# Kernel optimization log

Measured on AMD Instinct MI355X. Metric: run time of the kernel, lower is better.

Reference implementation:

```python
import jax, jax.numpy as jnp
import numpy as np

B, N, E, H, DEPTH = 2, 2048, 1024, 8, 12
D = E // H // 2  # head_dim = 64
LN_EPS = 1e-5


def setup_inputs() -> dict:
    key = jax.random.key(0)
    ks = jax.random.split(key, 10)
    w = lambda k: jax.random.normal(k, (E, E), jnp.float32) * (E ** -0.5)
    lp = lambda k: jax.random.normal(k, (D,), jnp.float32) * 0.1
    return {
        "x": jax.random.normal(ks[0], (B, N, E), jnp.float32),
        "Wq": w(ks[1]), "Wk": w(ks[2]), "Wv": w(ks[3]), "Wo": w(ks[4]),
        "lq1": lp(ks[5]), "lk1": lp(ks[6]), "lq2": lp(ks[7]), "lk2": lp(ks[8]),
        "ln_g": jnp.ones((2 * D,), jnp.float32),
        "ln_b": jnp.zeros((2 * D,), jnp.float32),
    }


def reference(x, Wq, Wk, Wv, Wo, lq1, lk1, lq2, lk2, ln_g, ln_b):
    b, n, e = x.shape
    lam_init = 0.8 - 0.6 * np.exp(-0.3 * DEPTH)  # lambda_init_fn(depth)
    # projections; split into 2H half-heads of dim D for q,k; H heads of dim 2D for v
    q = (x @ Wq).reshape(b, n, 2 * H, D).transpose(0, 2, 1, 3) * (D ** -0.5)  # [b,2H,n,D]
    k = (x @ Wk).reshape(b, n, 2 * H, D).transpose(0, 2, 1, 3)                # [b,2H,n,D]
    v = (x @ Wv).reshape(b, n, H, 2 * D).transpose(0, 2, 1, 3)                # [b,H,n,2D]
    scores = jnp.einsum('bhqd,bhkd->bhqk', q, k)                              # [b,2H,n,n]
    attn = jax.nn.softmax(scores, axis=-1).reshape(b, H, 2, n, n)
    lam = jnp.exp(jnp.sum(lq1 * lk1)) - jnp.exp(jnp.sum(lq2 * lk2)) + lam_init
    w_diff = attn[:, :, 0] - lam * attn[:, :, 1]                              # [b,H,n,n]
    o = jnp.einsum('bhqk,bhkd->bhqd', w_diff, v)                              # [b,H,n,2D]
    # per-head LayerNorm over channel dim 2D
    mu = o.mean(-1, keepdims=True)
    var = ((o - mu) ** 2).mean(-1, keepdims=True)
    o = (o - mu) * jax.lax.rsqrt(var + LN_EPS) * ln_g + ln_b
    o = o.transpose(0, 2, 1, 3).reshape(b, n, e)
    return o @ Wo
```

## Files before the change

### kernel.cpp

```cpp
#include <hip/hip_runtime.h>
#include <hip/hip_bf16.h>
#include <math.h>

#define B_ 2
#define N_ 2048
#define E_ 1024
#define H_ 8

typedef __attribute__((ext_vector_type(8))) short frag8;
typedef __attribute__((ext_vector_type(4))) float f32x4;
typedef __attribute__((ext_vector_type(16))) float f32x16;
typedef __attribute__((ext_vector_type(8))) unsigned short u16x8;

constexpr float LAM_INIT = 0.7836057665316245f;
constexpr float LOG2E = 1.4426950408889634f;
constexpr float EXP2_GUARD = -23.083120654f;

static __device__ __forceinline__ float fast_exp2(float x) {
#if __has_builtin(__builtin_amdgcn_exp2f)
  return __builtin_amdgcn_exp2f(x);
#else
  return exp2f(x);
#endif
}

static __device__ __forceinline__ ushort f2bf(float f) {
  union { float f; unsigned u; } v; v.f = f;
  unsigned r = (v.u + 0x7FFFu + ((v.u >> 16) & 1u)) >> 16;
  return (ushort)r;
}

static __device__ __forceinline__ unsigned pkbf(float a, float b) {
  __hip_bfloat162 h = __float22bfloat162_rn(make_float2(a, b));
  return *(unsigned*)&h;
}

static __device__ __forceinline__ void async16(const void* g, void* l) {
  __builtin_amdgcn_global_load_lds((const __attribute__((address_space(1))) void*)g,
                                   (__attribute__((address_space(3))) void*)l, 16, 0, 0);
}

static __device__ __forceinline__ frag8 mkfrag(unsigned p0, unsigned p1,
                                               unsigned p2, unsigned p3) {
  auto r02 = __builtin_amdgcn_permlane32_swap((int)p0, (int)p2, false, false);
  auto r13 = __builtin_amdgcn_permlane32_swap((int)p1, (int)p3, false, false);
  union { unsigned u[4]; frag8 f; } u;
  u.u[0] = (unsigned)r02[0];
  u.u[1] = (unsigned)r13[0];
  u.u[2] = (unsigned)r02[1];
  u.u[3] = (unsigned)r13[1];
  return u.f;
}

__global__ __launch_bounds__(256) void prep_kernel(
    const float* __restrict__ x,
    const float* __restrict__ Wq, const float* __restrict__ Wk,
    const float* __restrict__ Wv, const float* __restrict__ Wo,
    const float* __restrict__ lq1, const float* __restrict__ lk1,
    const float* __restrict__ lq2, const float* __restrict__ lk2,
    ushort* __restrict__ xb, ushort* __restrict__ wqkvt, ushort* __restrict__ wot,
    float* __restrict__ lam_out) {
  __shared__ ushort t[64][72];
  const int bx = blockIdx.x;
  const int tid = threadIdx.x;
  if (bx < 2048) {
    int i = bx * 256 + tid;
    const float4* sp = (const float4*)x + (size_t)i * 2;
    float4 a = sp[0], b = sp[1];
    u16x8 o;
    o[0] = f2bf(a.x); o[1] = f2bf(a.y); o[2] = f2bf(a.z); o[3] = f2bf(a.w);
    o[4] = f2bf(b.x); o[5] = f2bf(b.y); o[6] = f2bf(b.z); o[7] = f2bf(b.w);
    *(u16x8*)(xb + (size_t)i * 8) = o;
  } else if (bx < 3072) {
    int idx = bx - 2048;
    int sel = idx >> 8, rem = idx & 255;
    const float* W = (sel == 0) ? Wq : (sel == 1) ? Wk : (sel == 2) ? Wv : Wo;
    ushort* Wt = (sel < 3) ? (wqkvt + (size_t)sel * 1048576) : wot;
    const int c0 = (rem & 15) * 64, r0 = (rem >> 4) * 64;
    {
      int r = tid >> 2, cc = (tid & 3) * 16;
      const float* sp = W + (size_t)(r0 + r) * 1024 + c0 + cc;
      #pragma unroll
      for (int j = 0; j < 4; j++) {
        float4 a = *(const float4*)(sp + j * 4);
        t[cc + j * 4 + 0][r] = f2bf(a.x);
        t[cc + j * 4 + 1][r] = f2bf(a.y);
        t[cc + j * 4 + 2][r] = f2bf(a.z);
        t[cc + j * 4 + 3][r] = f2bf(a.w);
      }
    }
    __syncthreads();
    int c = tid >> 2, rr = (tid & 3) * 16;
    ushort* dp = Wt + (size_t)(c0 + c) * 1024 + r0 + rr;
    *(u16x8*)dp = *(u16x8*)&t[c][rr];
    *(u16x8*)(dp + 8) = *(u16x8*)&t[c][rr + 8];
  } else {
    if (tid < 64) {
      float t1 = lq1[tid] * lk1[tid];
      float t2 = lq2[tid] * lk2[tid];
      #pragma unroll
      for (int off = 32; off > 0; off >>= 1) {
        t1 += __shfl_down(t1, off);
        t2 += __shfl_down(t2, off);
      }
      if (tid == 0) lam_out[0] = expf(t1) - expf(t2) + LAM_INIT;
    }
  }
}

__global__ __launch_bounds__(512, 2) void gemm_qkv(const ushort* __restrict__ xb,
                                                   const ushort* __restrict__ wqkvt,
                                                   ushort* __restrict__ qkb,
                                                   ushort* __restrict__ vtb, float qscale) {
  __shared__ char smem[131072];
  const int id0 = blockIdx.x;
  const int id = (id0 & 7) * 24 + (id0 >> 3);
  const ushort* Ag; const ushort* Bg; ushort* C;
  int m0, n0, ldc;
  float sc;
  if (id < 128) {
    m0 = (id >> 3) * 256; n0 = (id & 7) * 256;
    Ag = xb; Bg = wqkvt; C = qkb; ldc = 2048;
    sc = (n0 < 1024) ? qscale : 1.0f;
  } else {
    int id2 = id - 128;
    m0 = (id2 & 3) * 256; n0 = (id2 >> 2) * 256;
    Ag = wqkvt + 2 * 1048576; Bg = xb; C = vtb; ldc = 4096;
    sc = 1.0f;
  }
  const int tid = threadIdx.x;
  const int w = tid >> 6, l = tid & 63;
  const int quad = l >> 4, col16 = l & 15;
  const int wr128 = (w >> 2) * 128;
  const int wc64 = (w & 3) * 64;

  f32x4 acc[8][4];
  #pragma unroll
  for (int mi = 0; mi < 8; mi++)
    #pragma unroll
    for (int nj = 0; nj < 4; nj++) acc[mi][nj] = (f32x4){0.f, 0.f, 0.f, 0.f};

  auto stage = [&](int kt, char* buf) {
    const int k0 = kt * 64;
    #pragma unroll
    for (int rr = 0; rr < 4; rr++) {
      int e = rr * 512 + tid;
      int row = e >> 3, slot = e & 7;
      int ksw = k0 + ((slot ^ (row & 7)) << 3);
      async16(Ag + (size_t)(m0 + row) * 1024 + ksw, buf + e * 16);
      async16(Bg + (size_t)(n0 + row) * 1024 + ksw, buf + 32768 + e * 16);
    }
  };

  auto compute = [&](const char* buf) {
    const char* Ab = buf;
    const char* Bb = buf + 32768;
    frag8 bf_[4][2];
    #pragma unroll
    for (int nj = 0; nj < 4; nj++) {
      int rb = wc64 + nj * 16 + col16;
      #pragma unroll
      for (int kk = 0; kk < 2; kk++) {
        int slot = kk * 4 + quad;
        bf_[nj][kk] = *(const frag8*)(Bb + rb * 128 + ((slot ^ (rb & 7)) << 4));
      }
    }
    __builtin_amdgcn_s_setprio(1);
    #pragma unroll
    for (int mi = 0; mi < 8; mi++) {
      int ra = wr128 + mi * 16 + col16;
      frag8 a0 = *(const frag8*)(Ab + ra * 128 + ((quad ^ (ra & 7)) << 4));
      frag8 a1 = *(const frag8*)(Ab + ra * 128 + (((4 + quad) ^ (ra & 7)) << 4));
      #pragma unroll
      for (int nj = 0; nj < 4; nj++) {
        acc[mi][nj] = __builtin_amdgcn_mfma_f32_16x16x32_bf16(a0, bf_[nj][0], acc[mi][nj], 0, 0, 0);
        acc[mi][nj] = __builtin_amdgcn_mfma_f32_16x16x32_bf16(a1, bf_[nj][1], acc[mi][nj], 0, 0, 0);
      }
    }
    __builtin_amdgcn_s_setprio(0);
  };

  char* buf0 = smem;
  char* buf1 = smem + 65536;
  stage(0, buf0);
  #pragma unroll 1
  for (int kt = 0; kt < 16; kt++) {
    char* cur = (kt & 1) ? buf1 : buf0;
    char* nxt = (kt & 1) ? buf0 : buf1;
    __syncthreads();
    if (kt < 15) stage(kt + 1, nxt);
    compute(cur);
  }

  #pragma unroll
  for (int mi = 0; mi < 8; mi++)
    #pragma unroll
    for (int r = 0; r < 4; r++) {
      int m = m0 + wr128 + mi * 16 + quad * 4 + r;
      #pragma unroll
      for (int nj = 0; nj < 4; nj++) {
        int n = n0 + wc64 + nj * 16 + col16;
        C[(size_t)m * ldc + n] = f2bf(acc[mi][nj][r] * sc);
      }
    }
}

__global__ __launch_bounds__(256) void gemm_out(const ushort* __restrict__ A,
                                                const ushort* __restrict__ Bt,
                                                float* __restrict__ Cp) {
  __shared__ ushort As[2048];
  __shared__ ushort Bs[4096];
  const int tid = threadIdx.x;
  const int w = tid >> 6, l = tid & 63;
  const int quad = l >> 4, col16 = l & 15;
  const int m0 = blockIdx.y * 64, n0 = blockIdx.x * 128;
  const int wm = (w & 1) * 32, wn = (w >> 1) * 64;
  const int lrow = l >> 2, lcol = (l & 3) * 8;

  f32x4 acc[2][4];
  #pragma unroll
  for (int mt = 0; mt < 2; mt++)
    #pragma unroll
    for (int nt = 0; nt < 4; nt++) acc[mt][nt] = (f32x4){0.f, 0.f, 0.f, 0.f};

  for (int k0 = 0; k0 < 1024; k0 += 32) {
    __syncthreads();
    #pragma unroll
    for (int i = 0; i < 3; i++) {
      int s = w * 3 + i;
      if (s < 4) {
        const ushort* gp = A + (size_t)(m0 + s * 16 + lrow) * 1024 + k0 + lcol;
        async16(gp, (char*)As + s * 1024);
      } else {
        int s2 = s - 4;
        const ushort* gp = Bt + (size_t)(n0 + s2 * 16 + lrow) * 1024 + k0 + lcol;
        async16(gp, (char*)Bs + s2 * 1024);
      }
    }
    __syncthreads();
    frag8 af[2], bfr[4];
    #pragma unroll
    for (int mt = 0; mt < 2; mt++)
      af[mt] = *(const frag8*)((const char*)As + (wm + mt * 16 + col16) * 64 + quad * 16);
    #pragma unroll
    for (int nt = 0; nt < 4; nt++)
      bfr[nt] = *(const frag8*)((const char*)Bs + (wn + nt * 16 + col16) * 64 + quad * 16);
    #pragma unroll
    for (int mt = 0; mt < 2; mt++)
      #pragma unroll
      for (int nt = 0; nt < 4; nt++)
        acc[mt][nt] = __builtin_amdgcn_mfma_f32_16x16x32_bf16(af[mt], bfr[nt], acc[mt][nt], 0, 0, 0);
  }

  #pragma unroll
  for (int mt = 0; mt < 2; mt++)
    #pragma unroll
    for (int r = 0; r < 4; r++) {
      int m = m0 + wm + mt * 16 + quad * 4 + r;
      #pragma unroll
      for (int nt = 0; nt < 4; nt++) {
        int n = n0 + wn + nt * 16 + col16;
        Cp[(size_t)m * 1024 + n] = acc[mt][nt][r];
      }
    }
}

__global__ __launch_bounds__(512, 2) void flash_kernel(const ushort* __restrict__ qk,
                                                       const ushort* __restrict__ vt,
                                                       const float* __restrict__ lam_p,
                                                       const float* __restrict__ ln_g,
                                                       const float* __restrict__ ln_b,
                                                       ushort* __restrict__ onorm) {
  const int L = blockIdx.x;
  const int hb = (L & 7) | (((L >> 3) & 1) << 3);
  const int qb = L >> 4;
  const int h = hb & 7, b = hb >> 3;

  const int tid = threadIdx.x;
  const int w = tid >> 6;
  const int hsel = w >> 2;
  const int h2 = 2 * h + hsel;
  const int lane31 = tid & 31, half = (tid & 63) >> 5;
  const int qloc = (w & 3) * 32 + lane31;
  const int i0 = qb * 128 + (w & 3) * 32;

  __shared__ char smem[131584];
  char* A0 = smem;
  char* A1 = smem + 32768;
  char* B0 = smem + 65536;
  char* B1 = smem + 98304;
  float* epi = (float*)smem;
  float* epi_l = (float*)(smem + 131072);

  const float lam = lam_p[0];

  frag8 qf[4];
  #pragma unroll
  for (int chk = 0; chk < 4; chk++) {
    const ushort* qp = qk + (size_t)(b * N_ + i0 + lane31) * 2048 +
                       h2 * 64 + chk * 16 + half * 8;
    qf[chk] = *(const frag8*)qp;
  }

  f32x16 o_[4];
  #pragma unroll
  for (int cm = 0; cm < 4; cm++)
    #pragma unroll
    for (int i = 0; i < 16; i++) o_[cm][i] = 0.f;
  float la0 = 0.f, la1 = 0.f;

  auto stage = [&](int k0, char* buf) {
    {
      int row = tid >> 3, sch = (tid & 7) ^ (row & 7);
      const ushort* kg = qk + (size_t)(b * N_ + k0 + row) * 2048 + 1024 + (2 * h) * 64 + sch * 8;
      async16(kg, buf + w * 1024);
    }
    {
      int row = tid >> 3, sch = (tid & 7) ^ (row & 7);
      const ushort* kg = qk + (size_t)(b * N_ + k0 + row) * 2048 + 1024 + (2 * h + 1) * 64 + sch * 8;
      async16(kg, buf + 8192 + w * 1024);
    }
    #pragma unroll
    for (int it = 0; it < 2; it++) {
      int j = it * 512 + tid;
      int row = j >> 3, sch = (j & 7) ^ (row & 7);
      const ushort* vg = vt + (size_t)(h * 128 + row) * 4096 + b * N_ + k0 + sch * 8;
      async16(vg, buf + 16384 + it * 8192 + w * 1024);
    }
  };

  auto compute = [&](const char* buf) {
    const char* Kb = buf + hsel * 8192;
    const char* Vb = buf + 16384;
    #pragma unroll
    for (int kh = 0; kh < 2; kh++) {
      f32x16 st;
      #pragma unroll
      for (int i = 0; i < 16; i++) st[i] = EXP2_GUARD;
      const int r = kh * 32 + lane31;
      __builtin_amdgcn_s_setprio(1);
      #pragma unroll
      for (int chk = 0; chk < 4; chk++) {
        frag8 a = *(const frag8*)(Kb + r * 128 + (((chk << 1) | half) ^ (r & 7)) * 16);
        st = __builtin_amdgcn_mfma_f32_32x32x16_bf16(a, qf[chk], st, 0, 0, 0);
      }
      __builtin_amdgcn_s_setprio(0);
      unsigned pk[8];
      #pragma unroll
      for (int p = 0; p < 8; p++) {
        float e0 = fast_exp2(st[2 * p]);
        float e1 = fast_exp2(st[2 * p + 1]);
        la0 += e0;
        la1 += e1;
        pk[p] = pkbf(e0, e1);
      }
      #pragma unroll
      for (int c16 = 0; c16 < 2; c16++) {
        frag8 bfr = mkfrag(pk[c16 * 4 + 0], pk[c16 * 4 + 1],
                           pk[c16 * 4 + 2], pk[c16 * 4 + 3]);
        __builtin_amdgcn_s_setprio(1);
        #pragma unroll
        for (int cm = 0; cm < 4; cm++) {
          int c = cm * 32 + lane31;
          int g = (kh * 4 + c16 * 2 + half) ^ (c & 7);
          frag8 a = *(const frag8*)(Vb + c * 128 + g * 16);
          o_[cm] = __builtin_amdgcn_mfma_f32_32x32x16_bf16(a, bfr, o_[cm], 0, 0, 0);
        }
        __builtin_amdgcn_s_setprio(0);
      }
    }
  };

  stage(0, A0);
  stage(64, A1);
  #pragma unroll 1
  for (int j = 0; j < 8; j++) {
    const int k0 = j * 256;
    __syncthreads();
    stage(k0 + 128, B0);
    stage(k0 + 192, B1);
    compute(A0);
    compute(A1);
    __syncthreads();
    if (j < 7) {
      stage(k0 + 256, A0);
      stage(k0 + 320, A1);
    }
    compute(B0);
    compute(B1);
  }

  float l_acc = la0 + la1;
  float lt = l_acc + __shfl_xor(l_acc, 32);

  if (hsel == 1) {
    if (half == 0) epi_l[qloc] = lt;
    #pragma unroll
    for (int cm = 0; cm < 4; cm++)
      #pragma unroll
      for (int g = 0; g < 4; g++) {
        int c = cm * 32 + g * 8 + half * 4;
        int pch = (c >> 2) ^ (qloc & 31);
        *(f32x4*)&epi[qloc * 128 + pch * 4] =
            (f32x4){o_[cm][4 * g + 0], o_[cm][4 * g + 1],
                    o_[cm][4 * g + 2], o_[cm][4 * g + 3]};
      }
  }
  __syncthreads();
  if (hsel == 0) {
    const float rle = 1.0f / lt;
    const float rlo = 1.0f / epi_l[qloc];
    float sum = 0.f, ss = 0.f;
    #pragma unroll
    for (int cm = 0; cm < 4; cm++)
      #pragma unroll
      for (int g = 0; g < 4; g++) {
        int c = cm * 32 + g * 8 + half * 4;
        int pch = (c >> 2) ^ (qloc & 31);
        f32x4 ov = *(const f32x4*)&epi[qloc * 128 + pch * 4];
        #pragma unroll
        for (int j = 0; j < 4; j++) {
          float v = o_[cm][4 * g + j] * rle - lam * ov[j] * rlo;
          o_[cm][4 * g + j] = v;
          sum += v;
          ss += v * v;
        }
      }
    sum += __shfl_xor(sum, 32);
    ss += __shfl_xor(ss, 32);
    float mu = sum * (1.0f / 128.0f);
    float var = ss * (1.0f / 128.0f) - mu * mu;
    float rr = rsqrtf(var + 1e-5f);
    int q = qb * 128 + qloc;
    ushort* ob = onorm + ((size_t)(b * N_ + q)) * E_ + h * 128;
    #pragma unroll
    for (int cm = 0; cm < 4; cm++)
      #pragma unroll
      for (int g = 0; g < 4; g++) {
        int c = cm * 32 + g * 8 + half * 4;
        float4 g4 = *(const float4*)&ln_g[c];
        float4 b4 = *(const float4*)&ln_b[c];
        float v0 = (o_[cm][4 * g + 0] - mu) * rr * g4.x + b4.x;
        float v1 = (o_[cm][4 * g + 1] - mu) * rr * g4.y + b4.y;
        float v2 = (o_[cm][4 * g + 2] - mu) * rr * g4.z + b4.z;
        float v3 = (o_[cm][4 * g + 3] - mu) * rr * g4.w + b4.w;
        uint2 pv;
        pv.x = pkbf(v0, v1);
        pv.y = pkbf(v2, v3);
        *(uint2*)(ob + c) = pv;
      }
  }
}

extern "C" void kernel_launch(void* const* d_in, const int* in_sizes, int n_in,
                              void* d_out, int out_size, void* d_ws, size_t ws_size,
                              hipStream_t stream) {
  const float* x    = (const float*)d_in[0];
  const float* Wq   = (const float*)d_in[1];
  const float* Wk   = (const float*)d_in[2];
  const float* Wv   = (const float*)d_in[3];
  const float* Wo   = (const float*)d_in[4];
  const float* lq1  = (const float*)d_in[5];
  const float* lk1  = (const float*)d_in[6];
  const float* lq2  = (const float*)d_in[7];
  const float* lk2  = (const float*)d_in[8];
  const float* ln_g = (const float*)d_in[9];
  const float* ln_b = (const float*)d_in[10];
  float* out = (float*)d_out;

  const size_t MN = (size_t)B_ * N_ * E_;
  ushort* xb    = (ushort*)d_ws;
  ushort* wqkvt = xb + MN;
  ushort* wot   = wqkvt + 3 * 1048576;
  ushort* qkb   = wot + 1048576;
  ushort* vtb   = qkb + (size_t)4096 * 2048;
  float*  lam   = (float*)(vtb + MN);
  ushort* onorm = xb;

  prep_kernel<<<dim3(3073), 256, 0, stream>>>(x, Wq, Wk, Wv, Wo, lq1, lk1, lq2, lk2,
                                              xb, wqkvt, wot, lam);

  gemm_qkv<<<dim3(192), 512, 0, stream>>>(xb, wqkvt, qkb, vtb, 0.125f * LOG2E);

  flash_kernel<<<dim3(256), 512, 0, stream>>>(qkb, vtb, lam, ln_g, ln_b, onorm);

  gemm_out<<<dim3(8, 64), 256, 0, stream>>>(onorm, wot, out);
}
```

Measured before the change: 207.7 us.

## Software-pipeline gemm_out with quad-buffered LDS and remap block order

After: 194.9 us, median of 2. 1.07x faster.

```diff
diff --git a/kernel.cpp b/kernel.cpp
--- a/kernel.cpp
+++ b/kernel.cpp
@@ -208,12 +208,13 @@
 __global__ __launch_bounds__(256) void gemm_out(const ushort* __restrict__ A,
                                                 const ushort* __restrict__ Bt,
                                                 float* __restrict__ Cp) {
-  __shared__ ushort As[2048];
-  __shared__ ushort Bs[4096];
+  __shared__ char smem[49152];
+  const int id0 = blockIdx.x;
+  const int id = (id0 & 7) * 64 + (id0 >> 3);
+  const int m0 = (id >> 3) * 64, n0 = (id & 7) * 128;
   const int tid = threadIdx.x;
   const int w = tid >> 6, l = tid & 63;
   const int quad = l >> 4, col16 = l & 15;
-  const int m0 = blockIdx.y * 64, n0 = blockIdx.x * 128;
   const int wm = (w & 1) * 32, wn = (w >> 1) * 64;
   const int lrow = l >> 2, lcol = (l & 3) * 8;
 
@@ -223,33 +224,63 @@
     #pragma unroll
     for (int nt = 0; nt < 4; nt++) acc[mt][nt] = (f32x4){0.f, 0.f, 0.f, 0.f};
 
-  for (int k0 = 0; k0 < 1024; k0 += 32) {
-    __syncthreads();
+  auto stage = [&](int kt, char* buf) {
+    const int k0 = kt * 32;
     #pragma unroll
     for (int i = 0; i < 3; i++) {
       int s = w * 3 + i;
       if (s < 4) {
         const ushort* gp = A + (size_t)(m0 + s * 16 + lrow) * 1024 + k0 + lcol;
-        async16(gp, (char*)As + s * 1024);
+        async16(gp, buf + s * 1024);
       } else {
         int s2 = s - 4;
         const ushort* gp = Bt + (size_t)(n0 + s2 * 16 + lrow) * 1024 + k0 + lcol;
-        async16(gp, (char*)Bs + s2 * 1024);
-      }
-    }
-    __syncthreads();
+        async16(gp, buf + 4096 + s2 * 1024);
+      }
+    }
+  };
+
+  auto compute = [&](const char* buf) {
+    const char* As_ = buf;
+    const char* Bs_ = buf + 4096;
     frag8 af[2], bfr[4];
     #pragma unroll
     for (int mt = 0; mt < 2; mt++)
-      af[mt] = *(const frag8*)((const char*)As + (wm + mt * 16 + col16) * 64 + quad * 16);
+      af[mt] = *(const frag8*)(As_ + (wm + mt * 16 + col16) * 64 + quad * 16);
     #pragma unroll
     for (int nt = 0; nt < 4; nt++)
-      bfr[nt] = *(const frag8*)((const char*)Bs + (wn + nt * 16 + col16) * 64 + quad * 16);
+      bfr[nt] = *(const frag8*)(Bs_ + (wn + nt * 16 + col16) * 64 + quad * 16);
+    __builtin_amdgcn_s_setprio(1);
     #pragma unroll
     for (int mt = 0; mt < 2; mt++)
       #pragma unroll
       for (int nt = 0; nt < 4; nt++)
         acc[mt][nt] = __builtin_amdgcn_mfma_f32_16x16x32_bf16(af[mt], bfr[nt], acc[mt][nt], 0, 0, 0);
+    __builtin_amdgcn_s_setprio(0);
+  };
+
+  char* P0 = smem;
+  char* P1 = smem + 12288;
+  char* P2 = smem + 24576;
+  char* P3 = smem + 36864;
+
+  stage(0, P0);
+  stage(1, P1);
+  #pragma unroll 1
+  for (int j = 0; j < 8; j++) {
+    const int t = j * 4;
+    __syncthreads();
+    stage(t + 2, P2);
+    stage(t + 3, P3);
+    compute(P0);
+    compute(P1);
+    __syncthreads();
+    if (j < 7) {
+      stage(t + 4, P0);
+      stage(t + 5, P1);
+    }
+    compute(P2);
+    compute(P3);
   }
 
   #pragma unroll
@@ -484,5 +515,5 @@
 
   flash_kernel<<<dim3(256), 512, 0, stream>>>(qkb, vtb, lam, ln_g, ln_b, onorm);
 
-  gemm_out<<<dim3(8, 64), 256, 0, stream>>>(onorm, wot, out);
-}
+  gemm_out<<<dim3(512), 256, 0, stream>>>(onorm, wot, out);
+}
```
